# Optimization experiments

Measured on AMD Instinct MI355X. Metric: run time of the kernel, lower is better.

## Reference

```python
import jax, jax.numpy as jnp
import numpy as np


def setup_inputs() -> dict:
    key = jax.random.key(0)
    k1, k2, k3, k4 = jax.random.split(key, 4)
    B, IN_DIM, OUT_DIM = 2048, 4096, 4096
    inputs = jax.random.normal(k1, (B, IN_DIM), dtype=jnp.float32)
    # integer weight code: each element of the implicit (in_dim,out_dim) weight
    # matrix is an index into the per-row `mean` vector of length in_dim
    indices = jax.random.randint(k2, (IN_DIM, OUT_DIM), 0, IN_DIM, dtype=jnp.int32)
    mean = jax.random.normal(k3, (IN_DIM,), dtype=jnp.float32)
    bias = jax.random.normal(k4, (OUT_DIM,), dtype=jnp.float32)
    return {"inputs": inputs, "indices": indices, "mean": mean, "bias": bias}


def reference(inputs, indices, mean, bias):
    # 'unsort' op: decode weight W[i,j] = mean[indices[i,j]], then x @ W
    W = mean[indices]                      # (in_dim, out_dim) gather-decode
    out = jnp.einsum("bi,io->bo", inputs, W)  # (batch, out_dim)
    return out + bias                      # channels_last bias add
```

## Files before the change

kernel.cpp:

```cpp
#include <hip/hip_runtime.h>
#include <hip/hip_bf16.h>


#define M_DIM 2048
#define K_DIM 4096
#define N_DIM 4096

#define BM 128
#define BN 256
#define BK 64
#define NT (K_DIM / BK)
#define LDSA_BYTES (BM * BK * 2)
#define LDSB_BYTES (BN * BK * 2)
#define LDS_TILE   (LDSA_BYTES + LDSB_BYTES)

typedef __attribute__((ext_vector_type(8))) short short8v;
typedef __attribute__((ext_vector_type(4))) float f32x4;

__device__ __forceinline__ unsigned short f2bf(float x) {
    unsigned u = __builtin_bit_cast(unsigned, x);
    u += 0x7fffu + ((u >> 16) & 1u);
    return (unsigned short)(u >> 16);
}

__device__ __forceinline__ void gload_lds16(const void* g, void* l) {
    __builtin_amdgcn_global_load_lds(
        (const __attribute__((address_space(1))) void*)(uintptr_t)g,
        (__attribute__((address_space(3))) void*)(uintptr_t)l, 16, 0, 0);
}

__global__ void convert_a_kernel(const float* __restrict__ A,
                                 unsigned short* __restrict__ Abf) {
    int i = blockIdx.x * blockDim.x + threadIdx.x;
    const float4 v = ((const float4*)A)[i];
    ushort4 o;
    o.x = f2bf(v.x); o.y = f2bf(v.y); o.z = f2bf(v.z); o.w = f2bf(v.w);
    ((ushort4*)Abf)[i] = o;
}

__global__ void decode_transpose_kernel(const int* __restrict__ idx,
                                        const float* __restrict__ mean,
                                        unsigned short* __restrict__ Wt) {
    __shared__ float smean[K_DIM];
    __shared__ unsigned short tile[64][65];
    const int t = threadIdx.x;
    for (int i = t; i < K_DIM; i += 256) smean[i] = mean[i];
    __syncthreads();

    const int k0 = blockIdx.y * 64;
    const int n0 = blockIdx.x * 64;
    const int rb = t >> 4;
    const int cb = (t & 15) * 4;

    #pragma unroll
    for (int i = 0; i < 4; ++i) {
        const int r = rb + i * 16;
        const int4 v = *(const int4*)&idx[(size_t)(k0 + r) * N_DIM + n0 + cb];
        tile[cb + 0][r] = f2bf(smean[v.x]);
        tile[cb + 1][r] = f2bf(smean[v.y]);
        tile[cb + 2][r] = f2bf(smean[v.z]);
        tile[cb + 3][r] = f2bf(smean[v.w]);
    }
    __syncthreads();

    #pragma unroll
    for (int i = 0; i < 4; ++i) {
        const int r = rb + i * 16;
        ushort4 o;
        o.x = tile[r][cb + 0];
        o.y = tile[r][cb + 1];
        o.z = tile[r][cb + 2];
        o.w = tile[r][cb + 3];
        *(ushort4*)&Wt[(size_t)(n0 + r) * K_DIM + k0 + cb] = o;
    }
}


#define VM6   asm volatile("s_waitcnt vmcnt(6)" ::: "memory")
#define VM0   asm volatile("s_waitcnt vmcnt(0)" ::: "memory")
#define LGKM0 asm volatile("s_waitcnt lgkmcnt(0)" ::: "memory")

#define STG6(buf, t) do {                           \
    const int ko_ = (t) * BK;                       \
    gload_lds16(sA0 + ko_, (buf) + lA0);            \
    gload_lds16(sA1 + ko_, (buf) + lA1);            \
    gload_lds16(sB0 + ko_, (buf) + lB0);            \
    gload_lds16(sB1 + ko_, (buf) + lB1);            \
    gload_lds16(sB2 + ko_, (buf) + lB2);            \
    gload_lds16(sB3 + ko_, (buf) + lB3);            \
} while (0)

#define READF(aS, bS, buf) do {                          \
    aS[0] = *(const short8v*)((buf) + rA0);              \
    aS[1] = *(const short8v*)((buf) + rA1);              \
    aS[2] = *(const short8v*)((buf) + rA2);              \
    aS[3] = *(const short8v*)((buf) + rA3);              \
    bS[0] = *(const short8v*)((buf) + rB0);              \
    bS[1] = *(const short8v*)((buf) + rB1);              \
    bS[2] = *(const short8v*)((buf) + rB2);              \
    bS[3] = *(const short8v*)((buf) + rB3);              \
    aS[4] = *(const short8v*)((buf) + rA0 + so1);        \
    aS[5] = *(const short8v*)((buf) + rA1 + so1);        \
    aS[6] = *(const short8v*)((buf) + rA2 + so1);        \
    aS[7] = *(const short8v*)((buf) + rA3 + so1);        \
    bS[4] = *(const short8v*)((buf) + rB0 + so1);        \
    bS[5] = *(const short8v*)((buf) + rB1 + so1);        \
    bS[6] = *(const short8v*)((buf) + rB2 + so1);        \
    bS[7] = *(const short8v*)((buf) + rB3 + so1);        \
} while (0)

#define MM1(aS, bS, ia, jb, i, j) \
    acc[i][j] = __builtin_amdgcn_mfma_f32_16x16x32_bf16(aS[ia], bS[jb], acc[i][j], 0, 0, 0)

#define MMALL(aS, bS) do {                                                           \
    MM1(aS,bS,0,0,0,0); MM1(aS,bS,0,1,0,1); MM1(aS,bS,0,2,0,2); MM1(aS,bS,0,3,0,3);  \
    MM1(aS,bS,1,0,1,0); MM1(aS,bS,1,1,1,1); MM1(aS,bS,1,2,1,2); MM1(aS,bS,1,3,1,3);  \
    MM1(aS,bS,2,0,2,0); MM1(aS,bS,2,1,2,1); MM1(aS,bS,2,2,2,2); MM1(aS,bS,2,3,2,3);  \
    MM1(aS,bS,3,0,3,0); MM1(aS,bS,3,1,3,1); MM1(aS,bS,3,2,3,2); MM1(aS,bS,3,3,3,3);  \
    MM1(aS,bS,4,4,0,0); MM1(aS,bS,4,5,0,1); MM1(aS,bS,4,6,0,2); MM1(aS,bS,4,7,0,3);  \
    MM1(aS,bS,5,4,1,0); MM1(aS,bS,5,5,1,1); MM1(aS,bS,5,6,1,2); MM1(aS,bS,5,7,1,3);  \
    MM1(aS,bS,6,4,2,0); MM1(aS,bS,6,5,2,1); MM1(aS,bS,6,6,2,2); MM1(aS,bS,6,7,2,3);  \
    MM1(aS,bS,7,4,3,0); MM1(aS,bS,7,5,3,1); MM1(aS,bS,7,6,3,2); MM1(aS,bS,7,7,3,3);  \
} while (0)

#define BODY(bufRd, bufSt, tstg, cA, cB, nA, nB) do {  \
    READF(nA, nB, bufRd);                              \
    STG6(bufSt, tstg);                                 \
    __builtin_amdgcn_s_setprio(1);                     \
    MMALL(cA, cB);                                     \
    __builtin_amdgcn_s_setprio(0);                     \
    LGKM0;                                             \
    VM6;                                               \
    __builtin_amdgcn_s_barrier();                      \
} while (0)

__global__ __launch_bounds__(512, 2) void gemm_kernel(
        const unsigned short* __restrict__ Abf,
        const unsigned short* __restrict__ Wt,
        const float* __restrict__ bias,
        float* __restrict__ C) {
    __shared__ __align__(128) char lds[3 * LDS_TILE];

    const int tid  = threadIdx.x;
    const int lane = tid & 63;
    const int w    = tid >> 6;
    const int wm   = w >> 2;
    const int wn   = w & 3;
    const int lr   = lane & 15;
    const int kq   = lane >> 4;

    const int bid = blockIdx.x;
    const int wg  = (bid & 7) * 32 + (bid >> 3);
    const int m0  = (wg >> 4) * BM;
    const int n0  = (wg & 15) * BN;

    const int pA0 = tid,        pA1 = 512 + tid;
    const int pB0 = tid,        pB1 = 512 + tid;
    const int pB2 = 1024 + tid, pB3 = 1536 + tid;
    const unsigned short* sA0 = Abf + (size_t)(m0 + (pA0 >> 3)) * K_DIM + 8 * ((pA0 & 7) ^ ((pA0 >> 3) & 7));
    const unsigned short* sA1 = Abf + (size_t)(m0 + (pA1 >> 3)) * K_DIM + 8 * ((pA1 & 7) ^ ((pA1 >> 3) & 7));
    const unsigned short* sB0 = Wt  + (size_t)(n0 + (pB0 >> 3)) * K_DIM + 8 * ((pB0 & 7) ^ ((pB0 >> 3) & 7));
    const unsigned short* sB1 = Wt  + (size_t)(n0 + (pB1 >> 3)) * K_DIM + 8 * ((pB1 & 7) ^ ((pB1 >> 3) & 7));
    const unsigned short* sB2 = Wt  + (size_t)(n0 + (pB2 >> 3)) * K_DIM + 8 * ((pB2 & 7) ^ ((pB2 >> 3) & 7));
    const unsigned short* sB3 = Wt  + (size_t)(n0 + (pB3 >> 3)) * K_DIM + 8 * ((pB3 & 7) ^ ((pB3 >> 3) & 7));
    const int lA0 = pA0 * 16,              lA1 = pA1 * 16;
    const int lB0 = LDSA_BYTES + pB0 * 16, lB1 = LDSA_BYTES + pB1 * 16;
    const int lB2 = LDSA_BYTES + pB2 * 16, lB3 = LDSA_BYTES + pB3 * 16;

    const int c0  = kq ^ (lr & 7);
    const int sc  = c0 * 16;
    const int so1 = ((c0 ^ 4) - c0) * 16;
    const int rA0 = (wm * 64 +  0 + lr) * 128 + sc;
    const int rA1 = (wm * 64 + 16 + lr) * 128 + sc;
    const int rA2 = (wm * 64 + 32 + lr) * 128 + sc;
    const int rA3 = (wm * 64 + 48 + lr) * 128 + sc;
    const int rB0 = LDSA_BYTES + (wn * 64 +  0 + lr) * 128 + sc;
    const int rB1 = LDSA_BYTES + (wn * 64 + 16 + lr) * 128 + sc;
    const int rB2 = LDSA_BYTES + (wn * 64 + 32 + lr) * 128 + sc;
    const int rB3 = LDSA_BYTES + (wn * 64 + 48 + lr) * 128 + sc;

    char* b0v = (char*)lds;
    char* b1v = (char*)lds + LDS_TILE;
    char* b2v = (char*)lds + 2 * LDS_TILE;

    f32x4 acc[4][4] = {};
    short8v aE[8], bE[8], aO[8], bO[8];

    STG6(b0v, 0);
    STG6(b1v, 1);
    STG6(b2v, 2);
    VM6;
    __builtin_amdgcn_s_barrier();
    READF(aE, bE, b0v);
    LGKM0;
    __builtin_amdgcn_s_barrier();

    for (int tt = 0; tt < 10; ++tt) {
        const int t = tt * 6;
        BODY(b1v, b0v, t + 3, aE, bE, aO, bO);
        BODY(b2v, b1v, t + 4, aO, bO, aE, bE);
        BODY(b0v, b2v, t + 5, aE, bE, aO, bO);
        BODY(b1v, b0v, t + 6, aO, bO, aE, bE);
        BODY(b2v, b1v, t + 7, aE, bE, aO, bO);
        BODY(b0v, b2v, t + 8, aO, bO, aE, bE);
    }
    BODY(b1v, b0v, 63, aE, bE, aO, bO);
    READF(aE, bE, b2v);
    __builtin_amdgcn_s_setprio(1);
    MMALL(aO, bO);
    __builtin_amdgcn_s_setprio(0);
    LGKM0;
    VM0;
    __builtin_amdgcn_s_barrier();
    READF(aO, bO, b0v);
    __builtin_amdgcn_s_setprio(1);
    MMALL(aE, bE);
    MMALL(aO, bO);
    __builtin_amdgcn_s_setprio(0);

    #pragma unroll
    for (int j = 0; j < 4; ++j) {
        const int n = n0 + wn * 64 + j * 16 + lr;
        const float bv = bias[n];
        #pragma unroll
        for (int i = 0; i < 4; ++i) {
            const int mb = m0 + wm * 64 + i * 16 + kq * 4;
            #pragma unroll
            for (int q = 0; q < 4; ++q)
                C[(size_t)(mb + q) * N_DIM + n] = acc[i][j][q] + bv;
        }
    }
}

extern "C" void kernel_launch(void* const* d_in, const int* in_sizes, int n_in,
                              void* d_out, int out_size, void* d_ws, size_t ws_size,
                              hipStream_t stream) {
    const float* inputs  = (const float*)d_in[0];
    const int*   indices = (const int*)  d_in[1];
    const float* mean    = (const float*)d_in[2];
    const float* bias    = (const float*)d_in[3];
    float* out = (float*)d_out;

    unsigned short* Abf = (unsigned short*)d_ws;
    unsigned short* Wt  = (unsigned short*)((char*)d_ws + (size_t)M_DIM * K_DIM * 2);

    convert_a_kernel<<<(M_DIM * K_DIM / 4) / 256, 256, 0, stream>>>(inputs, Abf);
    decode_transpose_kernel<<<dim3(N_DIM / 64, K_DIM / 64), 256, 0, stream>>>(indices, mean, Wt);
    gemm_kernel<<<256, 512, 0, stream>>>(Abf, Wt, bias, out);
}
```

Measured before the change: 208.8 us.

## Load A fragments directly from global into registers, stage only B in LDS

The A operand no longer goes through LDS. Each wave loads its A fragments straight from global memory into registers one tile ahead, while only the B tile is staged into a triple-buffered LDS ring. This cuts LDS capacity and LDS read traffic, and it drops the lgkmcnt wait per iteration. The cost is uncoalesced 16-byte global loads for A that are issued by every wave sharing the same rows (four waves per wm duplicate them), plus reliance on vmcnt ordering that now mixes register loads with LDS-direct loads.

```diff
diff --git a/kernel.cpp b/kernel.cpp
--- a/kernel.cpp
+++ b/kernel.cpp
@@ -10,9 +10,7 @@
 #define BN 256
 #define BK 64
 #define NT (K_DIM / BK)
-#define LDSA_BYTES (BM * BK * 2)
-#define LDSB_BYTES (BN * BK * 2)
-#define LDS_TILE   (LDSA_BYTES + LDSB_BYTES)
+#define TILE_B (BN * BK * 2)
 
 typedef __attribute__((ext_vector_type(8))) short short8v;
 typedef __attribute__((ext_vector_type(4))) float f32x4;
@@ -76,33 +74,33 @@
 }
 
 
-#define VM6   asm volatile("s_waitcnt vmcnt(6)" ::: "memory")
-#define VM0   asm volatile("s_waitcnt vmcnt(0)" ::: "memory")
-#define LGKM0 asm volatile("s_waitcnt lgkmcnt(0)" ::: "memory")
-
-#define STG6(buf, t) do {                           \
+#define VM4  asm volatile("s_waitcnt vmcnt(4)" ::: "memory")
+#define VM0  asm volatile("s_waitcnt vmcnt(0)" ::: "memory")
+
+#define STG4(buf, t) do {                           \
     const int ko_ = (t) * BK;                       \
-    gload_lds16(sA0 + ko_, (buf) + lA0);            \
-    gload_lds16(sA1 + ko_, (buf) + lA1);            \
     gload_lds16(sB0 + ko_, (buf) + lB0);            \
     gload_lds16(sB1 + ko_, (buf) + lB1);            \
     gload_lds16(sB2 + ko_, (buf) + lB2);            \
     gload_lds16(sB3 + ko_, (buf) + lB3);            \
 } while (0)
 
-#define READF(aS, bS, buf) do {                          \
-    aS[0] = *(const short8v*)((buf) + rA0);              \
-    aS[1] = *(const short8v*)((buf) + rA1);              \
-    aS[2] = *(const short8v*)((buf) + rA2);              \
-    aS[3] = *(const short8v*)((buf) + rA3);              \
+#define LOADA(dst, t) do {                                   \
+    dst[0] = *(const short8v*)(aP0 + (t) * 64);              \
+    dst[1] = *(const short8v*)(aP1 + (t) * 64);              \
+    dst[2] = *(const short8v*)(aP2 + (t) * 64);              \
+    dst[3] = *(const short8v*)(aP3 + (t) * 64);              \
+    dst[4] = *(const short8v*)(aP0 + (t) * 64 + 32);         \
+    dst[5] = *(const short8v*)(aP1 + (t) * 64 + 32);         \
+    dst[6] = *(const short8v*)(aP2 + (t) * 64 + 32);         \
+    dst[7] = *(const short8v*)(aP3 + (t) * 64 + 32);         \
+} while (0)
+
+#define READB(bS, buf) do {                              \
     bS[0] = *(const short8v*)((buf) + rB0);              \
     bS[1] = *(const short8v*)((buf) + rB1);              \
     bS[2] = *(const short8v*)((buf) + rB2);              \
     bS[3] = *(const short8v*)((buf) + rB3);              \
-    aS[4] = *(const short8v*)((buf) + rA0 + so1);        \
-    aS[5] = *(const short8v*)((buf) + rA1 + so1);        \
-    aS[6] = *(const short8v*)((buf) + rA2 + so1);        \
-    aS[7] = *(const short8v*)((buf) + rA3 + so1);        \
     bS[4] = *(const short8v*)((buf) + rB0 + so1);        \
     bS[5] = *(const short8v*)((buf) + rB1 + so1);        \
     bS[6] = *(const short8v*)((buf) + rB2 + so1);        \
@@ -123,15 +121,15 @@
     MM1(aS,bS,7,4,3,0); MM1(aS,bS,7,5,3,1); MM1(aS,bS,7,6,3,2); MM1(aS,bS,7,7,3,3);  \
 } while (0)
 
-#define BODY(bufRd, bufSt, tstg, cA, cB, nA, nB) do {  \
-    READF(nA, nB, bufRd);                              \
-    STG6(bufSt, tstg);                                 \
-    __builtin_amdgcn_s_setprio(1);                     \
-    MMALL(cA, cB);                                     \
-    __builtin_amdgcn_s_setprio(0);                     \
-    LGKM0;                                             \
-    VM6;                                               \
-    __builtin_amdgcn_s_barrier();                      \
+#define ITER(bufRd, bufSt, tnext, aCur, aNxt) do {  \
+    READB(bF, bufRd);                               \
+    LOADA(aNxt, (tnext));                           \
+    STG4(bufSt, (tnext) + 1);                       \
+    __builtin_amdgcn_s_setprio(1);                  \
+    MMALL(aCur, bF);                                \
+    __builtin_amdgcn_s_setprio(0);                  \
+    VM4;                                            \
+    __builtin_amdgcn_s_barrier();                   \
 } while (0)
 
 __global__ __launch_bounds__(512, 2) void gemm_kernel(
@@ -139,7 +137,7 @@
         const unsigned short* __restrict__ Wt,
         const float* __restrict__ bias,
         float* __restrict__ C) {
-    __shared__ __align__(128) char lds[3 * LDS_TILE];
+    __shared__ __align__(128) char lds[3 * TILE_B];
 
     const int tid  = threadIdx.x;
     const int lane = tid & 63;
@@ -154,68 +152,62 @@
     const int m0  = (wg >> 4) * BM;
     const int n0  = (wg & 15) * BN;
 
-    const int pA0 = tid,        pA1 = 512 + tid;
+    const unsigned short* aP0 = Abf + (size_t)(m0 + wm * 64 +  0 + lr) * K_DIM + kq * 8;
+    const unsigned short* aP1 = Abf + (size_t)(m0 + wm * 64 + 16 + lr) * K_DIM + kq * 8;
+    const unsigned short* aP2 = Abf + (size_t)(m0 + wm * 64 + 32 + lr) * K_DIM + kq * 8;
+    const unsigned short* aP3 = Abf + (size_t)(m0 + wm * 64 + 48 + lr) * K_DIM + kq * 8;
+
     const int pB0 = tid,        pB1 = 512 + tid;
     const int pB2 = 1024 + tid, pB3 = 1536 + tid;
-    const unsigned short* sA0 = Abf + (size_t)(m0 + (pA0 >> 3)) * K_DIM + 8 * ((pA0 & 7) ^ ((pA0 >> 3) & 7));
-    const unsigned short* sA1 = Abf + (size_t)(m0 + (pA1 >> 3)) * K_DIM + 8 * ((pA1 & 7) ^ ((pA1 >> 3) & 7));
-    const unsigned short* sB0 = Wt  + (size_t)(n0 + (pB0 >> 3)) * K_DIM + 8 * ((pB0 & 7) ^ ((pB0 >> 3) & 7));
-    const unsigned short* sB1 = Wt  + (size_t)(n0 + (pB1 >> 3)) * K_DIM + 8 * ((pB1 & 7) ^ ((pB1 >> 3) & 7));
-    const unsigned short* sB2 = Wt  + (size_t)(n0 + (pB2 >> 3)) * K_DIM + 8 * ((pB2 & 7) ^ ((pB2 >> 3) & 7));
-    const unsigned short* sB3 = Wt  + (size_t)(n0 + (pB3 >> 3)) * K_DIM + 8 * ((pB3 & 7) ^ ((pB3 >> 3) & 7));
-    const int lA0 = pA0 * 16,              lA1 = pA1 * 16;
-    const int lB0 = LDSA_BYTES + pB0 * 16, lB1 = LDSA_BYTES + pB1 * 16;
-    const int lB2 = LDSA_BYTES + pB2 * 16, lB3 = LDSA_BYTES + pB3 * 16;
+    const unsigned short* sB0 = Wt + (size_t)(n0 + (pB0 >> 3)) * K_DIM + 8 * ((pB0 & 7) ^ ((pB0 >> 3) & 7));
+    const unsigned short* sB1 = Wt + (size_t)(n0 + (pB1 >> 3)) * K_DIM + 8 * ((pB1 & 7) ^ ((pB1 >> 3) & 7));
+    const unsigned short* sB2 = Wt + (size_t)(n0 + (pB2 >> 3)) * K_DIM + 8 * ((pB2 & 7) ^ ((pB2 >> 3) & 7));
+    const unsigned short* sB3 = Wt + (size_t)(n0 + (pB3 >> 3)) * K_DIM + 8 * ((pB3 & 7) ^ ((pB3 >> 3) & 7));
+    const int lB0 = pB0 * 16, lB1 = pB1 * 16;
+    const int lB2 = pB2 * 16, lB3 = pB3 * 16;
 
     const int c0  = kq ^ (lr & 7);
     const int sc  = c0 * 16;
     const int so1 = ((c0 ^ 4) - c0) * 16;
-    const int rA0 = (wm * 64 +  0 + lr) * 128 + sc;
-    const int rA1 = (wm * 64 + 16 + lr) * 128 + sc;
-    const int rA2 = (wm * 64 + 32 + lr) * 128 + sc;
-    const int rA3 = (wm * 64 + 48 + lr) * 128 + sc;
-    const int rB0 = LDSA_BYTES + (wn * 64 +  0 + lr) * 128 + sc;
-    const int rB1 = LDSA_BYTES + (wn * 64 + 16 + lr) * 128 + sc;
-    const int rB2 = LDSA_BYTES + (wn * 64 + 32 + lr) * 128 + sc;
-    const int rB3 = LDSA_BYTES + (wn * 64 + 48 + lr) * 128 + sc;
+    const int rB0 = (wn * 64 +  0 + lr) * 128 + sc;
+    const int rB1 = (wn * 64 + 16 + lr) * 128 + sc;
+    const int rB2 = (wn * 64 + 32 + lr) * 128 + sc;
+    const int rB3 = (wn * 64 + 48 + lr) * 128 + sc;
 
     char* b0v = (char*)lds;
-    char* b1v = (char*)lds + LDS_TILE;
-    char* b2v = (char*)lds + 2 * LDS_TILE;
+    char* b1v = (char*)lds + TILE_B;
+    char* b2v = (char*)lds + 2 * TILE_B;
 
     f32x4 acc[4][4] = {};
-    short8v aE[8], bE[8], aO[8], bO[8];
-
-    STG6(b0v, 0);
-    STG6(b1v, 1);
-    STG6(b2v, 2);
-    VM6;
-    __builtin_amdgcn_s_barrier();
-    READF(aE, bE, b0v);
-    LGKM0;
+    short8v aE[8], aO[8], bF[8];
+
+    LOADA(aE, 0);
+    STG4(b0v, 0);
+    STG4(b1v, 1);
+    VM4;
     __builtin_amdgcn_s_barrier();
 
     for (int tt = 0; tt < 10; ++tt) {
         const int t = tt * 6;
-        BODY(b1v, b0v, t + 3, aE, bE, aO, bO);
-        BODY(b2v, b1v, t + 4, aO, bO, aE, bE);
-        BODY(b0v, b2v, t + 5, aE, bE, aO, bO);
-        BODY(b1v, b0v, t + 6, aO, bO, aE, bE);
-        BODY(b2v, b1v, t + 7, aE, bE, aO, bO);
-        BODY(b0v, b2v, t + 8, aO, bO, aE, bE);
-    }
-    BODY(b1v, b0v, 63, aE, bE, aO, bO);
-    READF(aE, bE, b2v);
+        ITER(b0v, b2v, t + 1, aE, aO);
+        ITER(b1v, b0v, t + 2, aO, aE);
+        ITER(b2v, b1v, t + 3, aE, aO);
+        ITER(b0v, b2v, t + 4, aO, aE);
+        ITER(b1v, b0v, t + 5, aE, aO);
+        ITER(b2v, b1v, t + 6, aO, aE);
+    }
+    ITER(b0v, b2v, 61, aE, aO);
+    ITER(b1v, b0v, 62, aO, aE);
+    READB(bF, b2v);
+    LOADA(aO, 63);
     __builtin_amdgcn_s_setprio(1);
-    MMALL(aO, bO);
+    MMALL(aE, bF);
     __builtin_amdgcn_s_setprio(0);
-    LGKM0;
     VM0;
     __builtin_amdgcn_s_barrier();
-    READF(aO, bO, b0v);
+    READB(bF, b0v);
     __builtin_amdgcn_s_setprio(1);
-    MMALL(aE, bE);
-    MMALL(aO, bO);
+    MMALL(aO, bF);
     __builtin_amdgcn_s_setprio(0);
 
     #pragma unroll
```

Result: slower. 299.3 us (+43.4%).
